# Kernel optimization log

Measured on AMD Instinct MI355X. Metric: run time of the kernel, lower is better.

## Reference

```python
import jax, jax.numpy as jnp
import numpy as np

B, S, D, H = 4, 2048, 1024, 16
DEPTH = D // H
NEG = -1e9


def setup_inputs() -> dict:
    key = jax.random.key(0)
    ks = jax.random.split(key, 9)
    scale = 1.0 / np.sqrt(D)
    x = jax.random.normal(ks[0], (B, S, D), dtype=jnp.float32)
    # causal additive mask: 1 where future positions (masked), 0 elsewhere
    mask = jnp.triu(jnp.ones((S, S), dtype=jnp.float32), k=1)[None, None, :, :]
    wq = jax.random.normal(ks[1], (D, D), dtype=jnp.float32) * scale
    bq = jnp.zeros((D,), dtype=jnp.float32)
    wk = jax.random.normal(ks[2], (D, D), dtype=jnp.float32) * scale
    bk = jnp.zeros((D,), dtype=jnp.float32)
    wv = jax.random.normal(ks[3], (D, D), dtype=jnp.float32) * scale
    bv = jnp.zeros((D,), dtype=jnp.float32)
    wo = jax.random.normal(ks[4], (D, D), dtype=jnp.float32) * scale
    bo = jnp.zeros((D,), dtype=jnp.float32)
    return {"x": x, "mask": mask, "wq": wq, "bq": bq, "wk": wk, "bk": bk,
            "wv": wv, "bv": bv, "wo": wo, "bo": bo}


def _split_heads(t):
    # [B, S, D] -> [B, H, S, depth]
    return t.reshape(B, S, H, DEPTH).transpose(0, 2, 1, 3)


def reference(x, mask, wq, bq, wk, bk, wv, bv, wo, bo):
    q = _split_heads(x @ wq.T + bq)
    k = _split_heads(x @ wk.T + bk)
    v = _split_heads(x @ wv.T + bv)
    scores = jnp.einsum('bhqd,bhkd->bhqk', q, k) / jnp.sqrt(jnp.float32(DEPTH))
    scores = scores + mask * NEG
    attn = jax.nn.softmax(scores, axis=-1)
    out = jnp.einsum('bhqk,bhkd->bhqd', attn, v)  # [B, H, S, depth]
    out = out.transpose(0, 2, 1, 3).reshape(B, S, D)
    return out @ wo.T + bo
```

## Files before the change

### kernel.cpp

```cpp
#include <hip/hip_runtime.h>
#include <hip/hip_bf16.h>
#include <stdint.h>

typedef __attribute__((ext_vector_type(8))) short short8;
typedef __attribute__((ext_vector_type(4))) float f32x4;
typedef __attribute__((ext_vector_type(16))) float f32x16;

#define AS1 __attribute__((address_space(1)))
#define AS3 __attribute__((address_space(3)))

constexpr int Bc = 4, Sc = 2048, Dc = 1024, Hc = 16;

__device__ __forceinline__ unsigned short f2b(float x) {
  __hip_bfloat16 h = __float2bfloat16(x);
  return *reinterpret_cast<unsigned short*>(&h);
}

__device__ __forceinline__ uint32_t cvtpk(float lo, float hi) {
  uint32_t r;
  asm("v_cvt_pk_bf16_f32 %0, %1, %2" : "=v"(r) : "v"(lo), "v"(hi));
  return r;
}

__device__ __forceinline__ void glds16(const void* g, void* l) {
  __builtin_amdgcn_global_load_lds((const AS1 uint32_t*)g, (AS3 uint32_t*)l, 16, 0, 0);
}

__global__ void cast_f32_bf16_x4(const float* __restrict__ in,
                                 unsigned short* __restrict__ out, int n4) {
  int i = blockIdx.x * blockDim.x + threadIdx.x;
  if (i >= n4) return;
  float4 a = ((const float4*)in)[i];
  ushort4 o;
  o.x = f2b(a.x); o.y = f2b(a.y); o.z = f2b(a.z); o.w = f2b(a.w);
  ((ushort4*)out)[i] = o;
}

__global__ void cast_w4(const float* __restrict__ wq, const float* __restrict__ wk,
                        const float* __restrict__ wv, const float* __restrict__ wo,
                        unsigned short* __restrict__ oq, unsigned short* __restrict__ ok,
                        unsigned short* __restrict__ ov, unsigned short* __restrict__ oo) {
  int which = blockIdx.y;
  const float* in = which == 0 ? wq : which == 1 ? wk : which == 2 ? wv : wo;
  unsigned short* out = which == 0 ? oq : which == 1 ? ok : which == 2 ? ov : oo;
  int i = blockIdx.x * blockDim.x + threadIdx.x;
  float4 a = ((const float4*)in)[i];
  ushort4 o;
  o.x = f2b(a.x); o.y = f2b(a.y); o.z = f2b(a.z); o.w = f2b(a.w);
  ((ushort4*)out)[i] = o;
}

template<int MODE>
__device__ __forceinline__ void gemm128_b32(
    const unsigned short* __restrict__ A, const unsigned short* __restrict__ W,
    const float* __restrict__ bias, void* __restrict__ outp,
    int m0, int n0, unsigned short* lA, unsigned short* lB)
{
  const int tid = threadIdx.x;
  const int w = tid >> 6, lane = tid & 63;
  const int g = lane >> 4, c = lane & 15;
  const int wr = w >> 1, wc = w & 1;

  f32x4 acc[4][4];
#pragma unroll
  for (int i = 0; i < 4; ++i)
#pragma unroll
    for (int j = 0; j < 4; ++j) acc[i][j] = f32x4{0.f, 0.f, 0.f, 0.f};

  const int srow = lane >> 2;
  const int schunk = (lane & 3) * 8;

  for (int k0 = 0; k0 < 1024; k0 += 32) {
#pragma unroll
    for (int i = 0; i < 2; ++i) {
      int row = i * 64 + w * 16 + srow;
      glds16(A + (size_t)(m0 + row) * 1024 + k0 + schunk,
             (char*)lA + i * 4096 + w * 1024);
      glds16(W + (size_t)(n0 + row) * 1024 + k0 + schunk,
             (char*)lB + i * 4096 + w * 1024);
    }
    __syncthreads();

    short8 aF[4], bF[4];
#pragma unroll
    for (int mt = 0; mt < 4; ++mt) {
      int row = wr * 64 + mt * 16 + c;
      aF[mt] = *(const short8*)&lA[row * 32 + g * 8];
    }
#pragma unroll
    for (int nt = 0; nt < 4; ++nt) {
      int row = wc * 64 + nt * 16 + c;
      bF[nt] = *(const short8*)&lB[row * 32 + g * 8];
    }
#pragma unroll
    for (int mt = 0; mt < 4; ++mt)
#pragma unroll
      for (int nt = 0; nt < 4; ++nt)
        acc[mt][nt] = __builtin_amdgcn_mfma_f32_16x16x32_bf16(aF[mt], bF[nt],
                                                              acc[mt][nt], 0, 0, 0);
    __syncthreads();
  }

#pragma unroll
  for (int mt = 0; mt < 4; ++mt) {
    int mg = m0 + wr * 64 + mt * 16 + 4 * g;
#pragma unroll
    for (int nt = 0; nt < 4; ++nt) {
      int ng = n0 + wc * 64 + nt * 16 + c;
      float bb_ = bias[ng];
      if constexpr (MODE == 0) {
        unsigned short* o = (unsigned short*)outp;
#pragma unroll
        for (int r = 0; r < 4; ++r)
          o[(size_t)(mg + r) * 1024 + ng] = f2b(acc[mt][nt][r] + bb_);
      } else if constexpr (MODE == 1) {
        unsigned short* o = (unsigned short*)outp;
        int bb = mg >> 11, s0 = mg & 2047;
        int hh = ng >> 6, dd = ng & 63;
        ushort4 pk;
        pk.x = f2b(acc[mt][nt][0] + bb_);
        pk.y = f2b(acc[mt][nt][1] + bb_);
        pk.z = f2b(acc[mt][nt][2] + bb_);
        pk.w = f2b(acc[mt][nt][3] + bb_);
        *(ushort4*)&o[(((size_t)bb * Hc + hh) * 64 + dd) * Sc + s0] = pk;
      } else {
        float* o = (float*)outp;
#pragma unroll
        for (int r = 0; r < 4; ++r)
          o[(size_t)(mg + r) * 1024 + ng] = acc[mt][nt][r] + bb_;
      }
    }
  }
}

template<int MODE>
__device__ __forceinline__ void gemm128_b64(
    const unsigned short* __restrict__ A, const unsigned short* __restrict__ W,
    const float* __restrict__ bias, void* __restrict__ outp,
    int m0, int n0, unsigned short* lA, unsigned short* lB)
{
  const int tid = threadIdx.x;
  const int w = tid >> 6, lane = tid & 63;
  const int g = lane >> 4, c = lane & 15;
  const int wr = w >> 1, wc = w & 1;

  f32x4 acc[4][4];
#pragma unroll
  for (int i = 0; i < 4; ++i)
#pragma unroll
    for (int j = 0; j < 4; ++j) acc[i][j] = f32x4{0.f, 0.f, 0.f, 0.f};

  const int lrow8 = lane >> 3;
  const int gslot = (lane & 7) ^ lrow8;

  const unsigned short* ap[4];
  const unsigned short* bp[4];
#pragma unroll
  for (int j = 0; j < 4; ++j) {
    int row = (j * 4 + w) * 8 + lrow8;
    ap[j] = A + (size_t)(m0 + row) * 1024 + gslot * 8;
    bp[j] = W + (size_t)(n0 + row) * 1024 + gslot * 8;
  }

  const int sl0 = (g ^ (c & 7)) << 4;
  const int sl1 = ((4 ^ g) ^ (c & 7)) << 4;
  const char* lA0 = (const char*)lA + (wr * 64 + c) * 128 + sl0;
  const char* lA1 = (const char*)lA + (wr * 64 + c) * 128 + sl1;
  const char* lB0 = (const char*)lB + (wc * 64 + c) * 128 + sl0;
  const char* lB1 = (const char*)lB + (wc * 64 + c) * 128 + sl1;

#define STAGE64                                             \
  do {                                                      \
    _Pragma("unroll")                                       \
    for (int j = 0; j < 4; ++j) {                           \
      glds16(ap[j], (char*)lA + (j * 4 + w) * 1024);        \
      glds16(bp[j], (char*)lB + (j * 4 + w) * 1024);        \
      ap[j] += 64; bp[j] += 64;                             \
    }                                                       \
  } while (0)

  STAGE64;
  for (int t = 0; t < 16; ++t) {
    asm volatile("s_waitcnt vmcnt(0)" ::: "memory");
    __builtin_amdgcn_s_barrier();
    asm volatile("" ::: "memory");

#pragma unroll
    for (int ks = 0; ks < 2; ++ks) {
      short8 aF[4], bF[4];
#pragma unroll
      for (int mt = 0; mt < 4; ++mt)
        aF[mt] = *(const short8*)((ks ? lA1 : lA0) + mt * 2048);
#pragma unroll
      for (int nt = 0; nt < 4; ++nt)
        bF[nt] = *(const short8*)((ks ? lB1 : lB0) + nt * 2048);
#pragma unroll
      for (int mt = 0; mt < 4; ++mt)
#pragma unroll
        for (int nt = 0; nt < 4; ++nt)
          acc[mt][nt] = __builtin_amdgcn_mfma_f32_16x16x32_bf16(
              aF[mt], bF[nt], acc[mt][nt], 0, 0, 0);
    }
    asm volatile("" ::: "memory");
    __builtin_amdgcn_s_barrier();
    asm volatile("" ::: "memory");
    if (t + 1 < 16) STAGE64;
  }
#undef STAGE64

#pragma unroll
  for (int mt = 0; mt < 4; ++mt) {
    int mg = m0 + wr * 64 + mt * 16 + 4 * g;
#pragma unroll
    for (int nt = 0; nt < 4; ++nt) {
      int ng = n0 + wc * 64 + nt * 16 + c;
      float bb_ = bias[ng];
      if constexpr (MODE == 2) {
        float* o = (float*)outp;
#pragma unroll
        for (int r = 0; r < 4; ++r)
          o[(size_t)(mg + r) * 1024 + ng] = acc[mt][nt][r] + bb_;
      } else {
        unsigned short* o = (unsigned short*)outp;
#pragma unroll
        for (int r = 0; r < 4; ++r)
          o[(size_t)(mg + r) * 1024 + ng] = f2b(acc[mt][nt][r] + bb_);
      }
    }
  }
}

__global__ __launch_bounds__(256) void qkv_gemm(
    const unsigned short* __restrict__ xb,
    const unsigned short* __restrict__ wqb, const unsigned short* __restrict__ wkb,
    const unsigned short* __restrict__ wvb,
    const float* __restrict__ bq, const float* __restrict__ bk,
    const float* __restrict__ bv,
    unsigned short* __restrict__ qo, unsigned short* __restrict__ ko,
    unsigned short* __restrict__ vto)
{
  __shared__ unsigned short lA[128 * 32], lB[128 * 32];
  int m0 = blockIdx.x * 128;
  int which = blockIdx.y >> 3;
  int n0 = (blockIdx.y & 7) * 128;
  if (which == 0)      gemm128_b32<0>(xb, wqb, bq, qo, m0, n0, lA, lB);
  else if (which == 1) gemm128_b32<0>(xb, wkb, bk, ko, m0, n0, lA, lB);
  else                 gemm128_b32<1>(xb, wvb, bv, vto, m0, n0, lA, lB);
}

__global__ __launch_bounds__(256) void out_gemm(
    const unsigned short* __restrict__ ao, const unsigned short* __restrict__ wob,
    const float* __restrict__ bo, float* __restrict__ out)
{
  __shared__ unsigned short lA[128 * 64], lB[128 * 64];
  gemm128_b64<2>(ao, wob, bo, out, blockIdx.x * 128, blockIdx.y * 128, lA, lB);
}

__global__ __launch_bounds__(256, 4) void attn_kernel(
    const unsigned short* __restrict__ qg, const unsigned short* __restrict__ kg,
    const unsigned short* __restrict__ vtg, unsigned short* __restrict__ ao)
{
  __shared__ unsigned short lK[2][64 * 64];
  __shared__ unsigned short lV[2][64 * 64];

  const int bh = blockIdx.x;
  const int qt = 15 - blockIdx.y;
  const int b = bh >> 4, h = bh & 15;
  const int tid = threadIdx.x, w = tid >> 6, lane = tid & 63;
  const int qr = lane & 31, hi = lane >> 5;
  const int qbase = qt * 128 + 32 * w;
  constexpr float CE = 0.125f * 1.44269504f;

  short8 qB[4];
  {
    const unsigned short* qp = qg + (size_t)(b * Sc + qbase + qr) * Dc + h * 64 + 8 * hi;
#pragma unroll
    for (int i = 0; i < 4; ++i)
      qB[i] = *(const short8*)(qp + 16 * i);
  }

  float m_ = -3e38f, lv = 0.f;
  f32x16 oT[2];
#pragma unroll
  for (int n = 0; n < 2; ++n)
#pragma unroll
    for (int r = 0; r < 16; ++r) oT[n][r] = 0.f;

  const int srow8 = lane >> 3;
  const int sslot = lane & 7;
  const unsigned short* kb_ = kg + (size_t)b * Sc * Dc + h * 64;
  const unsigned short* vb_ = vtg + (size_t)bh * 64 * Sc;

  auto stage = [&](int buf, int t) {
    const int kv0 = t * 64;
#pragma unroll
    for (int i = 0; i < 2; ++i) {
      int row = i * 32 + w * 8 + srow8;
      int gch = sslot ^ (row & 7);
      glds16(kb_ + (size_t)(kv0 + row) * Dc + gch * 8,
             (char*)lK[buf] + i * 4096 + w * 1024);
      glds16(vb_ + (size_t)row * Sc + kv0 + gch * 8,
             (char*)lV[buf] + i * 4096 + w * 1024);
    }
  };

  const int ntl = 2 * (qt + 1);
  stage(0, 0);
  asm volatile("s_waitcnt vmcnt(0)" ::: "memory");
  __builtin_amdgcn_s_barrier();
  asm volatile("" ::: "memory");

  for (int t = 0; t < ntl; ++t) {
    const int cur = t & 1;
    const int kv0 = t * 64;
    if (t + 1 < ntl) stage(cur ^ 1, t + 1);

    if (kv0 <= qbase + 31) {
      short8 kA[2][4];
#pragma unroll
      for (int kblk = 0; kblk < 2; ++kblk) {
        const int row = kblk * 32 + qr;
        const int swz = (row & 7) << 4;
#pragma unroll
        for (int i = 0; i < 4; ++i)
          kA[kblk][i] = *(const short8*)((const char*)lK[cur] + row * 128 +
                          (((2 * i + hi) * 16) ^ swz));
      }

      f32x16 sT[2];
      __builtin_amdgcn_s_setprio(1);
#pragma unroll
      for (int kblk = 0; kblk < 2; ++kblk) {
        f32x16 s;
#pragma unroll
        for (int r = 0; r < 16; ++r) s[r] = 0.f;
#pragma unroll
        for (int i = 0; i < 4; ++i)
          s = __builtin_amdgcn_mfma_f32_32x32x16_bf16(kA[kblk][i], qB[i],
                                                      s, 0, 0, 0);
        sT[kblk] = s;
      }
      __builtin_amdgcn_s_setprio(0);

      if (kv0 + 63 > qbase) {
        const int q = qbase + qr;
#pragma unroll
        for (int kblk = 0; kblk < 2; ++kblk)
#pragma unroll
          for (int r = 0; r < 16; ++r) {
            int k = kv0 + kblk * 32 + (r & 3) + 8 * (r >> 2) + 4 * hi;
            if (k > q) sT[kblk][r] = -1e30f;
          }
      }

      float mx;
      {
        float x0 = fmaxf(sT[0][0], sT[1][0]);
        float x1 = fmaxf(sT[0][1], sT[1][1]);
        float x2 = fmaxf(sT[0][2], sT[1][2]);
        float x3 = fmaxf(sT[0][3], sT[1][3]);
#pragma unroll
        for (int r = 4; r < 16; r += 4) {
          x0 = fmaxf(x0, fmaxf(sT[0][r + 0], sT[1][r + 0]));
          x1 = fmaxf(x1, fmaxf(sT[0][r + 1], sT[1][r + 1]));
          x2 = fmaxf(x2, fmaxf(sT[0][r + 2], sT[1][r + 2]));
          x3 = fmaxf(x3, fmaxf(sT[0][r + 3], sT[1][r + 3]));
        }
        mx = fmaxf(fmaxf(x0, x1), fmaxf(x2, x3));
        mx = fmaxf(mx, __shfl_xor(mx, 32));
      }

      if (!__all(mx <= m_ + 64.f)) {
        const float mo = m_;
        const float mn = fmaxf(mo, mx);
        const float sf = __builtin_amdgcn_exp2f((mo - mn) * CE);
        m_ = mn;
        lv *= sf;
#pragma unroll
        for (int n = 0; n < 2; ++n)
#pragma unroll
          for (int r = 0; r < 16; ++r) oT[n][r] *= sf;
      }
      const float mc = m_ * CE;
      {
        float s0 = 0.f, s1 = 0.f, s2 = 0.f, s3 = 0.f;
#pragma unroll
        for (int kblk = 0; kblk < 2; ++kblk)
#pragma unroll
          for (int r = 0; r < 16; r += 4) {
            float p0 = __builtin_amdgcn_exp2f(sT[kblk][r + 0] * CE - mc);
            float p1 = __builtin_amdgcn_exp2f(sT[kblk][r + 1] * CE - mc);
            float p2 = __builtin_amdgcn_exp2f(sT[kblk][r + 2] * CE - mc);
            float p3 = __builtin_amdgcn_exp2f(sT[kblk][r + 3] * CE - mc);
            sT[kblk][r + 0] = p0; sT[kblk][r + 1] = p1;
            sT[kblk][r + 2] = p2; sT[kblk][r + 3] = p3;
            s0 += p0; s1 += p1; s2 += p2; s3 += p3;
          }
        lv += (s0 + s1) + (s2 + s3);
      }

      short8 pB[4];
#pragma unroll
      for (int kblk = 0; kblk < 2; ++kblk) {
        uint32_t pk[4][2];
#pragma unroll
        for (int qp = 0; qp < 4; ++qp)
#pragma unroll
          for (int rp = 0; rp < 2; ++rp)
            pk[qp][rp] = cvtpk(sT[kblk][4 * qp + 2 * rp],
                               sT[kblk][4 * qp + 2 * rp + 1]);
#pragma unroll
        for (int m2 = 0; m2 < 2; ++m2) {
          uint32_t s0 = hi ? pk[2 * m2][0] : pk[2 * m2 + 1][0];
          uint32_t s1 = hi ? pk[2 * m2][1] : pk[2 * m2 + 1][1];
          uint32_t r0 = __shfl_xor(s0, 32);
          uint32_t r1 = __shfl_xor(s1, 32);
          uint32_t w0 = hi ? r0 : pk[2 * m2][0];
          uint32_t w1 = hi ? r1 : pk[2 * m2][1];
          uint32_t w2 = hi ? pk[2 * m2 + 1][0] : r0;
          uint32_t w3 = hi ? pk[2 * m2 + 1][1] : r1;
          uint32_t tmp[4] = { w0, w1, w2, w3 };
          pB[2 * kblk + m2] = *(const short8*)tmp;
        }
      }

      short8 vA[2][4];
#pragma unroll
      for (int n = 0; n < 2; ++n) {
        const int row = 32 * n + qr;
        const int swz = (row & 7) << 4;
#pragma unroll
        for (int m = 0; m < 4; ++m)
          vA[n][m] = *(const short8*)((const char*)lV[cur] + row * 128 +
                       (((2 * m + hi) * 16) ^ swz));
      }

      __builtin_amdgcn_s_setprio(1);
#pragma unroll
      for (int n = 0; n < 2; ++n)
#pragma unroll
        for (int m = 0; m < 4; ++m)
          oT[n] = __builtin_amdgcn_mfma_f32_32x32x16_bf16(
              vA[n][m], pB[m], oT[n], 0, 0, 0);
      __builtin_amdgcn_s_setprio(0);
    }

    asm volatile("s_waitcnt vmcnt(0)" ::: "memory");
    __builtin_amdgcn_s_barrier();
    asm volatile("" ::: "memory");
  }

  {
    float l = lv + __shfl_xor(lv, 32);
    float inv = 1.0f / l;
    const int qrow = qbase + qr;
    unsigned short* op = ao + (size_t)(b * Sc + qrow) * Dc + h * 64;
#pragma unroll
    for (int n = 0; n < 2; ++n)
#pragma unroll
      for (int rg = 0; rg < 4; ++rg) {
        ushort4 pkv;
        pkv.x = f2b(oT[n][4 * rg + 0] * inv);
        pkv.y = f2b(oT[n][4 * rg + 1] * inv);
        pkv.z = f2b(oT[n][4 * rg + 2] * inv);
        pkv.w = f2b(oT[n][4 * rg + 3] * inv);
        *(ushort4*)(op + 32 * n + 8 * rg + 4 * hi) = pkv;
      }
  }
}

extern "C" void kernel_launch(void* const* d_in, const int* in_sizes, int n_in,
                              void* d_out, int out_size, void* d_ws, size_t ws_size,
                              hipStream_t stream) {
  const float* x  = (const float*)d_in[0];
  const float* wq = (const float*)d_in[2];
  const float* bq = (const float*)d_in[3];
  const float* wk = (const float*)d_in[4];
  const float* bk = (const float*)d_in[5];
  const float* wv = (const float*)d_in[6];
  const float* bv = (const float*)d_in[7];
  const float* wo = (const float*)d_in[8];
  const float* bo = (const float*)d_in[9];
  float* out = (float*)d_out;

  char* ws = (char*)d_ws;
  unsigned short* xb  = (unsigned short*)(ws);
  unsigned short* wqb = (unsigned short*)(ws + 16777216);
  unsigned short* wkb = (unsigned short*)(ws + 18874368);
  unsigned short* wvb = (unsigned short*)(ws + 20971520);
  unsigned short* wob = (unsigned short*)(ws + 23068672);
  unsigned short* qb  = (unsigned short*)(ws + 25165824);
  unsigned short* kb  = (unsigned short*)(ws + 41943040);
  unsigned short* vtb = (unsigned short*)(ws + 58720256);
  unsigned short* aob = (unsigned short*)(ws + 75497472);

  cast_f32_bf16_x4<<<8192, 256, 0, stream>>>(x, xb, 2097152);
  cast_w4<<<dim3(1024, 4), 256, 0, stream>>>(wq, wk, wv, wo, wqb, wkb, wvb, wob);

  qkv_gemm<<<dim3(64, 24), 256, 0, stream>>>(xb, wqb, wkb, wvb, bq, bk, bv,
                                             qb, kb, vtb);
  attn_kernel<<<dim3(64, 16), 256, 0, stream>>>(qb, kb, vtb, aob);
  out_gemm<<<dim3(64, 8), 256, 0, stream>>>(aob, wob, bo, out);
}
```

Before: 164.4 us.

## Load K/V tiles directly from global into registers, drop LDS staging

The attention kernel no longer double-buffers K and V tiles through shared memory with block barriers. Each wave now reads its K and V fragments straight from global memory, relying on L1/L2 caching. Each wave also runs its own causal tile count, so waves no longer wait for each other. This removes LDS traffic and barrier stalls, but the four waves of a block fetch the same K/V data redundantly and global-load latency is no longer hidden by prefetching.

```diff
diff --git a/kernel.cpp b/kernel.cpp
--- a/kernel.cpp
+++ b/kernel.cpp
@@ -260,9 +260,6 @@
     const unsigned short* __restrict__ qg, const unsigned short* __restrict__ kg,
     const unsigned short* __restrict__ vtg, unsigned short* __restrict__ ao)
 {
-  __shared__ unsigned short lK[2][64 * 64];
-  __shared__ unsigned short lV[2][64 * 64];
-
   const int bh = blockIdx.x;
   const int qt = 15 - blockIdx.y;
   const int b = bh >> 4, h = bh & 15;
@@ -286,168 +283,131 @@
 #pragma unroll
     for (int r = 0; r < 16; ++r) oT[n][r] = 0.f;
 
-  const int srow8 = lane >> 3;
-  const int sslot = lane & 7;
   const unsigned short* kb_ = kg + (size_t)b * Sc * Dc + h * 64;
   const unsigned short* vb_ = vtg + (size_t)bh * 64 * Sc;
 
-  auto stage = [&](int buf, int t) {
+  const int ntlw = 2 * qt + 1 + (w >> 1);
+
+  for (int t = 0; t < ntlw; ++t) {
     const int kv0 = t * 64;
-#pragma unroll
-    for (int i = 0; i < 2; ++i) {
-      int row = i * 32 + w * 8 + srow8;
-      int gch = sslot ^ (row & 7);
-      glds16(kb_ + (size_t)(kv0 + row) * Dc + gch * 8,
-             (char*)lK[buf] + i * 4096 + w * 1024);
-      glds16(vb_ + (size_t)row * Sc + kv0 + gch * 8,
-             (char*)lV[buf] + i * 4096 + w * 1024);
-    }
-  };
-
-  const int ntl = 2 * (qt + 1);
-  stage(0, 0);
-  asm volatile("s_waitcnt vmcnt(0)" ::: "memory");
-  __builtin_amdgcn_s_barrier();
-  asm volatile("" ::: "memory");
-
-  for (int t = 0; t < ntl; ++t) {
-    const int cur = t & 1;
-    const int kv0 = t * 64;
-    if (t + 1 < ntl) stage(cur ^ 1, t + 1);
-
-    if (kv0 <= qbase + 31) {
-      short8 kA[2][4];
-#pragma unroll
-      for (int kblk = 0; kblk < 2; ++kblk) {
-        const int row = kblk * 32 + qr;
-        const int swz = (row & 7) << 4;
-#pragma unroll
-        for (int i = 0; i < 4; ++i)
-          kA[kblk][i] = *(const short8*)((const char*)lK[cur] + row * 128 +
-                          (((2 * i + hi) * 16) ^ swz));
+
+    f32x16 sT[2];
+#pragma unroll
+    for (int kblk = 0; kblk < 2; ++kblk) {
+      const unsigned short* kp =
+          kb_ + (size_t)(kv0 + kblk * 32 + qr) * 1024 + 8 * hi;
+      short8 kA[4];
+#pragma unroll
+      for (int i = 0; i < 4; ++i)
+        kA[i] = *(const short8*)(kp + 16 * i);
+      f32x16 s;
+#pragma unroll
+      for (int r = 0; r < 16; ++r) s[r] = 0.f;
+      __builtin_amdgcn_s_setprio(1);
+#pragma unroll
+      for (int i = 0; i < 4; ++i)
+        s = __builtin_amdgcn_mfma_f32_32x32x16_bf16(kA[i], qB[i], s, 0, 0, 0);
+      __builtin_amdgcn_s_setprio(0);
+      sT[kblk] = s;
+    }
+
+    if (kv0 + 63 > qbase) {
+      const int q = qbase + qr;
+#pragma unroll
+      for (int kblk = 0; kblk < 2; ++kblk)
+#pragma unroll
+        for (int r = 0; r < 16; ++r) {
+          int k = kv0 + kblk * 32 + (r & 3) + 8 * (r >> 2) + 4 * hi;
+          if (k > q) sT[kblk][r] = -1e30f;
+        }
+    }
+
+    float mx;
+    {
+      float x0 = fmaxf(sT[0][0], sT[1][0]);
+      float x1 = fmaxf(sT[0][1], sT[1][1]);
+      float x2 = fmaxf(sT[0][2], sT[1][2]);
+      float x3 = fmaxf(sT[0][3], sT[1][3]);
+#pragma unroll
+      for (int r = 4; r < 16; r += 4) {
+        x0 = fmaxf(x0, fmaxf(sT[0][r + 0], sT[1][r + 0]));
+        x1 = fmaxf(x1, fmaxf(sT[0][r + 1], sT[1][r + 1]));
+        x2 = fmaxf(x2, fmaxf(sT[0][r + 2], sT[1][r + 2]));
+        x3 = fmaxf(x3, fmaxf(sT[0][r + 3], sT[1][r + 3]));
       }
-
-      f32x16 sT[2];
+      mx = fmaxf(fmaxf(x0, x1), fmaxf(x2, x3));
+      mx = fmaxf(mx, __shfl_xor(mx, 32));
+    }
+
+    if (!__all(mx <= m_ + 64.f)) {
+      const float mo = m_;
+      const float mn = fmaxf(mo, mx);
+      const float sf = __builtin_amdgcn_exp2f((mo - mn) * CE);
+      m_ = mn;
+      lv *= sf;
+#pragma unroll
+      for (int n = 0; n < 2; ++n)
+#pragma unroll
+        for (int r = 0; r < 16; ++r) oT[n][r] *= sf;
+    }
+    const float mc = m_ * CE;
+    {
+      float s0 = 0.f, s1 = 0.f, s2 = 0.f, s3 = 0.f;
+#pragma unroll
+      for (int kblk = 0; kblk < 2; ++kblk)
+#pragma unroll
+        for (int r = 0; r < 16; r += 4) {
+          float p0 = __builtin_amdgcn_exp2f(sT[kblk][r + 0] * CE - mc);
+          float p1 = __builtin_amdgcn_exp2f(sT[kblk][r + 1] * CE - mc);
+          float p2 = __builtin_amdgcn_exp2f(sT[kblk][r + 2] * CE - mc);
+          float p3 = __builtin_amdgcn_exp2f(sT[kblk][r + 3] * CE - mc);
+          sT[kblk][r + 0] = p0; sT[kblk][r + 1] = p1;
+          sT[kblk][r + 2] = p2; sT[kblk][r + 3] = p3;
+          s0 += p0; s1 += p1; s2 += p2; s3 += p3;
+        }
+      lv += (s0 + s1) + (s2 + s3);
+    }
+
+    short8 pB[4];
+#pragma unroll
+    for (int kblk = 0; kblk < 2; ++kblk) {
+      uint32_t pk[4][2];
+#pragma unroll
+      for (int qp = 0; qp < 4; ++qp)
+#pragma unroll
+        for (int rp = 0; rp < 2; ++rp)
+          pk[qp][rp] = cvtpk(sT[kblk][4 * qp + 2 * rp],
+                             sT[kblk][4 * qp + 2 * rp + 1]);
+#pragma unroll
+      for (int m2 = 0; m2 < 2; ++m2) {
+        uint32_t s0 = hi ? pk[2 * m2][0] : pk[2 * m2 + 1][0];
+        uint32_t s1 = hi ? pk[2 * m2][1] : pk[2 * m2 + 1][1];
+        uint32_t r0 = __shfl_xor(s0, 32);
+        uint32_t r1 = __shfl_xor(s1, 32);
+        uint32_t w0 = hi ? r0 : pk[2 * m2][0];
+        uint32_t w1 = hi ? r1 : pk[2 * m2][1];
+        uint32_t w2 = hi ? pk[2 * m2 + 1][0] : r0;
+        uint32_t w3 = hi ? pk[2 * m2 + 1][1] : r1;
+        uint32_t tmp[4] = { w0, w1, w2, w3 };
+        pB[2 * kblk + m2] = *(const short8*)tmp;
+      }
+    }
+
+#pragma unroll
+    for (int n = 0; n < 2; ++n) {
+      const unsigned short* vp =
+          vb_ + (size_t)(32 * n + qr) * 2048 + kv0 + 8 * hi;
+      short8 vA[4];
+#pragma unroll
+      for (int m = 0; m < 4; ++m)
+        vA[m] = *(const short8*)(vp + 16 * m);
       __builtin_amdgcn_s_setprio(1);
 #pragma unroll
-      for (int kblk = 0; kblk < 2; ++kblk) {
-        f32x16 s;
-#pragma unroll
-        for (int r = 0; r < 16; ++r) s[r] = 0.f;
-#pragma unroll
-        for (int i = 0; i < 4; ++i)
-          s = __builtin_amdgcn_mfma_f32_32x32x16_bf16(kA[kblk][i], qB[i],
-                                                      s, 0, 0, 0);
-        sT[kblk] = s;
-      }
+      for (int m = 0; m < 4; ++m)
+        oT[n] = __builtin_amdgcn_mfma_f32_32x32x16_bf16(
+            vA[m], pB[m], oT[n], 0, 0, 0);
       __builtin_amdgcn_s_setprio(0);
-
-      if (kv0 + 63 > qbase) {
-        const int q = qbase + qr;
-#pragma unroll
-        for (int kblk = 0; kblk < 2; ++kblk)
-#pragma unroll
-          for (int r = 0; r < 16; ++r) {
-            int k = kv0 + kblk * 32 + (r & 3) + 8 * (r >> 2) + 4 * hi;
-            if (k > q) sT[kblk][r] = -1e30f;
-          }
-      }
-
-      float mx;
-      {
-        float x0 = fmaxf(sT[0][0], sT[1][0]);
-        float x1 = fmaxf(sT[0][1], sT[1][1]);
-        float x2 = fmaxf(sT[0][2], sT[1][2]);
-        float x3 = fmaxf(sT[0][3], sT[1][3]);
-#pragma unroll
-        for (int r = 4; r < 16; r += 4) {
-          x0 = fmaxf(x0, fmaxf(sT[0][r + 0], sT[1][r + 0]));
-          x1 = fmaxf(x1, fmaxf(sT[0][r + 1], sT[1][r + 1]));
-          x2 = fmaxf(x2, fmaxf(sT[0][r + 2], sT[1][r + 2]));
-          x3 = fmaxf(x3, fmaxf(sT[0][r + 3], sT[1][r + 3]));
-        }
-        mx = fmaxf(fmaxf(x0, x1), fmaxf(x2, x3));
-        mx = fmaxf(mx, __shfl_xor(mx, 32));
-      }
-
-      if (!__all(mx <= m_ + 64.f)) {
-        const float mo = m_;
-        const float mn = fmaxf(mo, mx);
-        const float sf = __builtin_amdgcn_exp2f((mo - mn) * CE);
-        m_ = mn;
-        lv *= sf;
-#pragma unroll
-        for (int n = 0; n < 2; ++n)
-#pragma unroll
-          for (int r = 0; r < 16; ++r) oT[n][r] *= sf;
-      }
-      const float mc = m_ * CE;
-      {
-        float s0 = 0.f, s1 = 0.f, s2 = 0.f, s3 = 0.f;
-#pragma unroll
-        for (int kblk = 0; kblk < 2; ++kblk)
-#pragma unroll
-          for (int r = 0; r < 16; r += 4) {
-            float p0 = __builtin_amdgcn_exp2f(sT[kblk][r + 0] * CE - mc);
-            float p1 = __builtin_amdgcn_exp2f(sT[kblk][r + 1] * CE - mc);
-            float p2 = __builtin_amdgcn_exp2f(sT[kblk][r + 2] * CE - mc);
-            float p3 = __builtin_amdgcn_exp2f(sT[kblk][r + 3] * CE - mc);
-            sT[kblk][r + 0] = p0; sT[kblk][r + 1] = p1;
-            sT[kblk][r + 2] = p2; sT[kblk][r + 3] = p3;
-            s0 += p0; s1 += p1; s2 += p2; s3 += p3;
-          }
-        lv += (s0 + s1) + (s2 + s3);
-      }
-
-      short8 pB[4];
-#pragma unroll
-      for (int kblk = 0; kblk < 2; ++kblk) {
-        uint32_t pk[4][2];
-#pragma unroll
-        for (int qp = 0; qp < 4; ++qp)
-#pragma unroll
-          for (int rp = 0; rp < 2; ++rp)
-            pk[qp][rp] = cvtpk(sT[kblk][4 * qp + 2 * rp],
-                               sT[kblk][4 * qp + 2 * rp + 1]);
-#pragma unroll
-        for (int m2 = 0; m2 < 2; ++m2) {
-          uint32_t s0 = hi ? pk[2 * m2][0] : pk[2 * m2 + 1][0];
-          uint32_t s1 = hi ? pk[2 * m2][1] : pk[2 * m2 + 1][1];
-          uint32_t r0 = __shfl_xor(s0, 32);
-          uint32_t r1 = __shfl_xor(s1, 32);
-          uint32_t w0 = hi ? r0 : pk[2 * m2][0];
-          uint32_t w1 = hi ? r1 : pk[2 * m2][1];
-          uint32_t w2 = hi ? pk[2 * m2 + 1][0] : r0;
-          uint32_t w3 = hi ? pk[2 * m2 + 1][1] : r1;
-          uint32_t tmp[4] = { w0, w1, w2, w3 };
-          pB[2 * kblk + m2] = *(const short8*)tmp;
-        }
-      }
-
-      short8 vA[2][4];
-#pragma unroll
-      for (int n = 0; n < 2; ++n) {
-        const int row = 32 * n + qr;
-        const int swz = (row & 7) << 4;
-#pragma unroll
-        for (int m = 0; m < 4; ++m)
-          vA[n][m] = *(const short8*)((const char*)lV[cur] + row * 128 +
-                       (((2 * m + hi) * 16) ^ swz));
-      }
-
-      __builtin_amdgcn_s_setprio(1);
-#pragma unroll
-      for (int n = 0; n < 2; ++n)
-#pragma unroll
-        for (int m = 0; m < 4; ++m)
-          oT[n] = __builtin_amdgcn_mfma_f32_32x32x16_bf16(
-              vA[n][m], pB[m], oT[n], 0, 0, 0);
-      __builtin_amdgcn_s_setprio(0);
-    }
-
-    asm volatile("s_waitcnt vmcnt(0)" ::: "memory");
-    __builtin_amdgcn_s_barrier();
-    asm volatile("" ::: "memory");
+    }
   }
 
   {
```

After: 244.3 us. 48.6% more time.

## Fuse x fp32-to-bf16 cast into QKV GEMM A-tile loads

Applied to the files above, without the earlier changes.

Removes the separate kernel that casts x to bf16. The QKV GEMM now loads fp32 x tiles straight into LDS through a XOR-swizzled layout and converts them to bf16 in registers with v_cvt_pk_bf16_f32 before the MFMAs. This saves one kernel launch and the bf16 x round trip through memory. In exchange each of the 24 column-block groups rereads x in fp32, so the A-tile global traffic doubles, the LDS A tile doubles in size, and extra conversion instructions land in the inner loop. The staging loop is also reorganised to issue the next tile's loads after the second barrier, using pointer increments.

```diff
diff --git a/kernel.cpp b/kernel.cpp
--- a/kernel.cpp
+++ b/kernel.cpp
@@ -24,16 +24,6 @@
 
 __device__ __forceinline__ void glds16(const void* g, void* l) {
   __builtin_amdgcn_global_load_lds((const AS1 uint32_t*)g, (AS3 uint32_t*)l, 16, 0, 0);
-}
-
-__global__ void cast_f32_bf16_x4(const float* __restrict__ in,
-                                 unsigned short* __restrict__ out, int n4) {
-  int i = blockIdx.x * blockDim.x + threadIdx.x;
-  if (i >= n4) return;
-  float4 a = ((const float4*)in)[i];
-  ushort4 o;
-  o.x = f2b(a.x); o.y = f2b(a.y); o.z = f2b(a.z); o.w = f2b(a.w);
-  ((ushort4*)out)[i] = o;
 }
 
 __global__ void cast_w4(const float* __restrict__ wq, const float* __restrict__ wk,
@@ -51,10 +41,10 @@
 }
 
 template<int MODE>
-__device__ __forceinline__ void gemm128_b32(
-    const unsigned short* __restrict__ A, const unsigned short* __restrict__ W,
+__device__ __forceinline__ void gemm128_xf32(
+    const float* __restrict__ A, const unsigned short* __restrict__ W,
     const float* __restrict__ bias, void* __restrict__ outp,
-    int m0, int n0, unsigned short* lA, unsigned short* lB)
+    int m0, int n0, float* lA, unsigned short* lB)
 {
   const int tid = threadIdx.x;
   const int w = tid >> 6, lane = tid & 63;
@@ -67,25 +57,51 @@
 #pragma unroll
     for (int j = 0; j < 4; ++j) acc[i][j] = f32x4{0.f, 0.f, 0.f, 0.f};
 
+  const int arow8 = lane >> 3;
+  const int ach = (lane & 7) ^ arow8;
+  const float* ap[4];
+#pragma unroll
+  for (int i = 0; i < 2; ++i)
+#pragma unroll
+    for (int j = 0; j < 2; ++j)
+      ap[i * 2 + j] = A + (size_t)(m0 + i * 64 + w * 16 + j * 8 + arow8) * 1024 + ach * 4;
+
   const int srow = lane >> 2;
   const int schunk = (lane & 3) * 8;
-
-  for (int k0 = 0; k0 < 1024; k0 += 32) {
-#pragma unroll
-    for (int i = 0; i < 2; ++i) {
-      int row = i * 64 + w * 16 + srow;
-      glds16(A + (size_t)(m0 + row) * 1024 + k0 + schunk,
-             (char*)lA + i * 4096 + w * 1024);
-      glds16(W + (size_t)(n0 + row) * 1024 + k0 + schunk,
-             (char*)lB + i * 4096 + w * 1024);
-    }
+  const unsigned short* b0 = W + (size_t)(n0 + w * 16 + srow) * 1024 + schunk;
+  const unsigned short* b1 = b0 + (size_t)64 * 1024;
+
+#define STAGEX                                                        \
+  do {                                                                \
+    _Pragma("unroll")                                                 \
+    for (int i = 0; i < 2; ++i)                                       \
+      _Pragma("unroll")                                               \
+      for (int j = 0; j < 2; ++j) {                                   \
+        glds16(ap[i * 2 + j],                                         \
+               (char*)lA + (i * 64 + w * 16 + j * 8) * 128);          \
+        ap[i * 2 + j] += 32;                                          \
+      }                                                               \
+    glds16(b0, (char*)lB + w * 1024);                                 \
+    glds16(b1, (char*)lB + 4096 + w * 1024);                          \
+    b0 += 32; b1 += 32;                                               \
+  } while (0)
+
+  const int as1 = ((2 * g) ^ (c & 7)) * 16;
+  const int as2 = ((2 * g + 1) ^ (c & 7)) * 16;
+
+  STAGEX;
+  for (int t = 0; t < 32; ++t) {
     __syncthreads();
 
     short8 aF[4], bF[4];
 #pragma unroll
     for (int mt = 0; mt < 4; ++mt) {
       int row = wr * 64 + mt * 16 + c;
-      aF[mt] = *(const short8*)&lA[row * 32 + g * 8];
+      f32x4 a0 = *(const f32x4*)((const char*)lA + row * 128 + as1);
+      f32x4 a1 = *(const f32x4*)((const char*)lA + row * 128 + as2);
+      uint32_t u[4] = { cvtpk(a0[0], a0[1]), cvtpk(a0[2], a0[3]),
+                        cvtpk(a1[0], a1[1]), cvtpk(a1[2], a1[3]) };
+      aF[mt] = *(const short8*)u;
     }
 #pragma unroll
     for (int nt = 0; nt < 4; ++nt) {
@@ -99,7 +115,9 @@
         acc[mt][nt] = __builtin_amdgcn_mfma_f32_16x16x32_bf16(aF[mt], bF[nt],
                                                               acc[mt][nt], 0, 0, 0);
     __syncthreads();
-  }
+    if (t + 1 < 32) STAGEX;
+  }
+#undef STAGEX
 
 #pragma unroll
   for (int mt = 0; mt < 4; ++mt) {
@@ -113,7 +131,7 @@
 #pragma unroll
         for (int r = 0; r < 4; ++r)
           o[(size_t)(mg + r) * 1024 + ng] = f2b(acc[mt][nt][r] + bb_);
-      } else if constexpr (MODE == 1) {
+      } else {
         unsigned short* o = (unsigned short*)outp;
         int bb = mg >> 11, s0 = mg & 2047;
         int hh = ng >> 6, dd = ng & 63;
@@ -123,11 +141,6 @@
         pk.z = f2b(acc[mt][nt][2] + bb_);
         pk.w = f2b(acc[mt][nt][3] + bb_);
         *(ushort4*)&o[(((size_t)bb * Hc + hh) * 64 + dd) * Sc + s0] = pk;
-      } else {
-        float* o = (float*)outp;
-#pragma unroll
-        for (int r = 0; r < 4; ++r)
-          o[(size_t)(mg + r) * 1024 + ng] = acc[mt][nt][r] + bb_;
       }
     }
   }
@@ -231,7 +244,7 @@
 }
 
 __global__ __launch_bounds__(256) void qkv_gemm(
-    const unsigned short* __restrict__ xb,
+    const float* __restrict__ x,
     const unsigned short* __restrict__ wqb, const unsigned short* __restrict__ wkb,
     const unsigned short* __restrict__ wvb,
     const float* __restrict__ bq, const float* __restrict__ bk,
@@ -239,13 +252,14 @@
     unsigned short* __restrict__ qo, unsigned short* __restrict__ ko,
     unsigned short* __restrict__ vto)
 {
-  __shared__ unsigned short lA[128 * 32], lB[128 * 32];
+  __shared__ float lA[128 * 32];
+  __shared__ unsigned short lB[128 * 32];
   int m0 = blockIdx.x * 128;
   int which = blockIdx.y >> 3;
   int n0 = (blockIdx.y & 7) * 128;
-  if (which == 0)      gemm128_b32<0>(xb, wqb, bq, qo, m0, n0, lA, lB);
-  else if (which == 1) gemm128_b32<0>(xb, wkb, bk, ko, m0, n0, lA, lB);
-  else                 gemm128_b32<1>(xb, wvb, bv, vto, m0, n0, lA, lB);
+  if (which == 0)      gemm128_xf32<0>(x, wqb, bq, qo, m0, n0, lA, lB);
+  else if (which == 1) gemm128_xf32<0>(x, wkb, bk, ko, m0, n0, lA, lB);
+  else                 gemm128_xf32<1>(x, wvb, bv, vto, m0, n0, lA, lB);
 }
 
 __global__ __launch_bounds__(256) void out_gemm(
@@ -484,7 +498,6 @@
   float* out = (float*)d_out;
 
   char* ws = (char*)d_ws;
-  unsigned short* xb  = (unsigned short*)(ws);
   unsigned short* wqb = (unsigned short*)(ws + 16777216);
   unsigned short* wkb = (unsigned short*)(ws + 18874368);
   unsigned short* wvb = (unsigned short*)(ws + 20971520);
@@ -494,10 +507,9 @@
   unsigned short* vtb = (unsigned short*)(ws + 58720256);
   unsigned short* aob = (unsigned short*)(ws + 75497472);
 
-  cast_f32_bf16_x4<<<8192, 256, 0, stream>>>(x, xb, 2097152);
   cast_w4<<<dim3(1024, 4), 256, 0, stream>>>(wq, wk, wv, wo, wqb, wkb, wvb, wob);
 
-  qkv_gemm<<<dim3(64, 24), 256, 0, stream>>>(xb, wqb, wkb, wvb, bq, bk, bv,
+  qkv_gemm<<<dim3(64, 24), 256, 0, stream>>>(x, wqb, wkb, wvb, bq, bk, bv,
                                              qb, kb, vtb);
   attn_kernel<<<dim3(64, 16), 256, 0, stream>>>(qb, kb, vtb, aob);
   out_gemm<<<dim3(64, 8), 256, 0, stream>>>(aob, wob, bo, out);
```

Result: slower. 178.8 us (+8.8%).
